# Performance work log

Hardware: AMD Instinct MI355X
Metric: run time of the kernel (lower is better)

## Reference

```python
import jax, jax.numpy as jnp
import numpy as np

BBOX_MIN = jnp.array([0.6, 0.6, 0.2], dtype=jnp.float32)
BBOX_MAX = jnp.array([-0.8, -1.2, -0.2], dtype=jnp.float32)
# level resolutions: floor(16 * (4096/16)**(l/15)) for l in 0..4
RES = [16, 23, 33, 48, 70]
OFFS = np.cumsum([0] + [(r + 1) ** 3 for r in RES]).tolist()  # dense grids fit in 2^21 hashmap


def _encode(x, table):
    # x: [N,3] in [0,1]; table: [533601, 2] concatenated dense per-level grids
    feats = []
    for l, r in enumerate(RES):
        g = r + 1  # grid points per axis
        pos = x * r
        p0 = jnp.clip(jnp.floor(pos), 0.0, r - 1)
        f = pos - p0  # trilinear weights, [N,3]
        p0 = p0.astype(jnp.int32)
        acc = jnp.zeros((x.shape[0], 2), dtype=table.dtype)
        for dx in (0, 1):
            for dy in (0, 1):
                for dz in (0, 1):
                    idx = ((p0[:, 0] + dx) * g + (p0[:, 1] + dy)) * g + (p0[:, 2] + dz) + OFFS[l]
                    wx = f[:, 0] if dx else 1.0 - f[:, 0]
                    wy = f[:, 1] if dy else 1.0 - f[:, 1]
                    wz = f[:, 2] if dz else 1.0 - f[:, 2]
                    acc = acc + (wx * wy * wz)[:, None] * table[idx]
        feats.append(acc)
    return jnp.concatenate(feats, axis=-1)  # [N, 10]


def setup_inputs() -> dict:
    key = jax.random.key(0)
    ks = jax.random.split(key, 5)
    T = OFFS[-1]  # 533601
    return {
        "texc": jax.random.uniform(ks[0], (2048, 2048, 3), dtype=jnp.float32),
        "table": jax.random.normal(ks[1], (T, 2), dtype=jnp.float32) * 1e-4,
        "W0": jax.random.normal(ks[2], (32, 10), dtype=jnp.float32) * (2.0 / 10) ** 0.5,
        "W1": jax.random.normal(ks[3], (32, 32), dtype=jnp.float32) * (2.0 / 32) ** 0.5,
        "W2": jax.random.normal(ks[4], (3, 32), dtype=jnp.float32) * (2.0 / 32) ** 0.5,
        "min_val": jnp.zeros((3,), jnp.float32),
        "max_val": jnp.ones((3,), jnp.float32),
        "frame_id": 0,
    }


def reference(texc, table, W0, W1, W2, min_val, max_val, frame_id):
    x = texc.reshape(-1, 3)
    # coordinate normalization into [0,1] with hardcoded bbox (as in source)
    x = jnp.clip((x - BBOX_MIN) / (BBOX_MAX - BBOX_MIN), 0.0, 1.0)
    p = _encode(x, table)              # [N, 10]
    h = jax.nn.relu(p @ W0.T)          # [N, 32]
    h = jax.nn.relu(h @ W1.T)          # [N, 32]
    o = h @ W2.T                       # [N, 3]
    o = jax.nn.sigmoid(o) * (max_val - min_val) + min_val
    return o.reshape(*texc.shape[:-1], 3)
```

## Files before the change

kernel.cpp:

```cpp
#include <hip/hip_runtime.h>
#include <hip/hip_bf16.h>
#include <math.h>


namespace {

typedef __attribute__((ext_vector_type(8)))  short short8;
typedef __attribute__((ext_vector_type(16))) float f32x16;
typedef __attribute__((ext_vector_type(4), aligned(8))) float f32x4a;
typedef __attribute__((ext_vector_type(4), aligned(16))) unsigned int u32x4;

union S8 { short8 v; int d[4]; };

#define SWAP32(a, b) asm volatile("v_permlane32_swap_b32 %0, %1" : "+v"(a), "+v"(b))

constexpr int RES0 = 16, RES1 = 23, RES2 = 33, RES3 = 48, RES4 = 70;
constexpr int TOFF0 = 0, TOFF1 = 4913, TOFF2 = 18737, TOFF3 = 58041, TOFF4 = 175690;
constexpr int COFF0 = 0;
constexpr int COFF1 = COFF0 + RES0*RES0*RES0;
constexpr int COFF2 = COFF1 + RES1*RES1*RES1;
constexpr int COFF3 = COFF2 + RES2*RES2*RES2;
constexpr int COFF4 = COFF3 + RES3*RES3*RES3;
constexpr int NCELL = COFF4 + RES4*RES4*RES4;
constexpr size_t WS_NEED = (size_t)NCELL * 32u;

__device__ __forceinline__ int cvt_pk(float lo, float hi) {
    int d;
    asm("v_cvt_pk_bf16_f32 %0, %1, %2" : "=v"(d) : "v"(lo), "v"(hi));
    return d;
}

__device__ __forceinline__ short8 pack8(float4 a, float4 b) {
    S8 u;
    u.d[0] = cvt_pk(a.x, a.y);
    u.d[1] = cvt_pk(a.z, a.w);
    u.d[2] = cvt_pk(b.x, b.y);
    u.d[3] = cvt_pk(b.z, b.w);
    return u.v;
}

__device__ __forceinline__ float clamp01(float v) {
    return fminf(fmaxf(v, 0.0f), 1.0f);
}

__device__ __forceinline__ float2 upk(unsigned int u) {
    float2 r;
    r.x = __uint_as_float(u << 16);
    r.y = __uint_as_float(u & 0xffff0000u);
    return r;
}

__device__ __forceinline__ void marshal_h(const f32x16& acc, short8& k0, short8& k1) {
    int q[8];
    #pragma unroll
    for (int j = 0; j < 8; ++j) {
        float lo = fmaxf(acc[2*j],   0.0f);
        float hi = fmaxf(acc[2*j+1], 0.0f);
        q[j] = cvt_pk(lo, hi);
    }
    int a0 = q[0], b0 = q[2]; SWAP32(a0, b0);
    int a1 = q[1], b1 = q[3]; SWAP32(a1, b1);
    int a2 = q[4], b2 = q[6]; SWAP32(a2, b2);
    int a3 = q[5], b3 = q[7]; SWAP32(a3, b3);
    S8 u0; u0.d[0] = a0; u0.d[1] = a1; u0.d[2] = b0; u0.d[3] = b1; k0 = u0.v;
    S8 u1; u1.d[0] = a2; u1.d[1] = a3; u1.d[2] = b2; u1.d[3] = b3; k1 = u1.v;
}

__global__ __launch_bounds__(256) void prep_kernel(
    const float* __restrict__ table, unsigned int* __restrict__ ws)
{
    int ci = blockIdx.x * blockDim.x + threadIdx.x;
    if (ci >= NCELL) return;

    int r, toff, c0;
    if      (ci < COFF1) { r = RES0; toff = TOFF0; c0 = COFF0; }
    else if (ci < COFF2) { r = RES1; toff = TOFF1; c0 = COFF1; }
    else if (ci < COFF3) { r = RES2; toff = TOFF2; c0 = COFF2; }
    else if (ci < COFF4) { r = RES3; toff = TOFF3; c0 = COFF3; }
    else                 { r = RES4; toff = TOFF4; c0 = COFF4; }

    int lc = ci - c0;
    int cz = lc % r;
    int t  = lc / r;
    int cy = t % r;
    int cx = t / r;
    int g  = r + 1;

    const float2* tab2 = reinterpret_cast<const float2*>(table);
    int base = (cx * g + cy) * g + cz + toff;

    unsigned int* dst = ws + (size_t)ci * 8;
    #pragma unroll
    for (int dx = 0; dx < 2; ++dx) {
        #pragma unroll
        for (int dy = 0; dy < 2; ++dy) {
            #pragma unroll
            for (int dz = 0; dz < 2; ++dz) {
                float2 v = tab2[base + (dx * g + dy) * g + dz];
                dst[dx*4 + dy*2 + dz] = (unsigned int)cvt_pk(v.x, v.y);
            }
        }
    }
}

template<bool USE_WS>
__global__ __launch_bounds__(512) void mlptex_kernel(
    const float* __restrict__ texc,
    const float* __restrict__ table,
    const unsigned int* __restrict__ cells,
    const float* __restrict__ W0,
    const float* __restrict__ W1,
    const float* __restrict__ W2,
    const float* __restrict__ minv,
    const float* __restrict__ maxv,
    float* __restrict__ out,
    int N)
{
    const int tid  = blockIdx.x * blockDim.x + threadIdx.x;
    const int lane = threadIdx.x & 63;
    const int pt   = min(tid, N - 1);
    const bool live = (tid < N);

    const int row = lane & 31;
    const int kb  = lane >> 5;

    short8 w0f, w1f0, w1f1;
    {
        const float* p0 = W0 + row * 10;
        float4 a, b;
        if (kb == 0) {
            float2 f0 = *(const float2*)(p0 + 0);
            float2 f1 = *(const float2*)(p0 + 2);
            float2 f2 = *(const float2*)(p0 + 4);
            float2 f3 = *(const float2*)(p0 + 6);
            a = make_float4(f0.x, f0.y, f1.x, f1.y);
            b = make_float4(f2.x, f2.y, f3.x, f3.y);
        } else {
            float2 f4 = *(const float2*)(p0 + 8);
            a = make_float4(f4.x, f4.y, 0.f, 0.f);
            b = make_float4(0.f, 0.f, 0.f, 0.f);
        }
        w0f = pack8(a, b);

        const float* p1 = W1 + row * 32 + kb * 8;
        w1f0 = pack8(*(const float4*)(p1),      *(const float4*)(p1 + 4));
        w1f1 = pack8(*(const float4*)(p1 + 16), *(const float4*)(p1 + 20));
    }
    short8 w2f0 = {0,0,0,0,0,0,0,0}, w2f1 = {0,0,0,0,0,0,0,0};
    if (row < 3) {
        const float* p2 = W2 + row * 32 + kb * 8;
        w2f0 = pack8(*(const float4*)(p2),      *(const float4*)(p2 + 4));
        w2f1 = pack8(*(const float4*)(p2 + 16), *(const float4*)(p2 + 20));
    }

    const float* tp = texc + 3 * pt;
    float x = __builtin_nontemporal_load(tp + 0);
    float y = __builtin_nontemporal_load(tp + 1);
    float z = __builtin_nontemporal_load(tp + 2);
    x = clamp01((x - 0.6f) * (-1.0f/1.4f));
    y = clamp01((y - 0.6f) * (-1.0f/1.8f));
    z = clamp01((z - 0.2f) * (-1.0f/0.4f));

    const int RESL[5]  = {RES0, RES1, RES2, RES3, RES4};
    const int TOFFL[5] = {TOFF0, TOFF1, TOFF2, TOFF3, TOFF4};
    const int COFFL[5] = {COFF0, COFF1, COFF2, COFF3, COFF4};
    const float2* tab2 = reinterpret_cast<const float2*>(table);

    float pf[10];
    #pragma unroll
    for (int l = 0; l < 5; ++l) {
        const int r = RESL[l];
        const int g = r + 1;
        const float rf = (float)r;
        float px = x * rf, py = y * rf, pz = z * rf;
        float fx = fminf(floorf(px), rf - 1.0f);
        float fy = fminf(floorf(py), rf - 1.0f);
        float fz = fminf(floorf(pz), rf - 1.0f);
        float tx = px - fx, ty = py - fy, tz = pz - fz;
        int ix = (int)fx & 127, iy = (int)fy & 127, iz = (int)fz & 127;

        float sx = 1.0f - tx, sy = 1.0f - ty, sz = 1.0f - tz;
        float w00 = sy*sz, w01 = sy*tz, w10 = ty*sz, w11 = ty*tz;
        float a00 = sx*w00, a01 = sx*w01, a10 = sx*w10, a11 = sx*w11;
        float b00 = tx*w00, b01 = tx*w01, b10 = tx*w10, b11 = tx*w11;

        float f0, f1;
        if constexpr (USE_WS) {
            int ci = (ix * r + iy) * r + iz + COFFL[l];
            const u32x4* cp = reinterpret_cast<const u32x4*>(cells + (size_t)ci * 8);
            u32x4 lo = cp[0];
            u32x4 hi = cp[1];
            float2 c000 = upk(lo.x), c001 = upk(lo.y), c010 = upk(lo.z), c011 = upk(lo.w);
            float2 c100 = upk(hi.x), c101 = upk(hi.y), c110 = upk(hi.z), c111 = upk(hi.w);
            f0  = a00*c000.x;            f1  = a00*c000.y;
            f0  = fmaf(a01, c001.x, f0); f1  = fmaf(a01, c001.y, f1);
            f0  = fmaf(a10, c010.x, f0); f1  = fmaf(a10, c010.y, f1);
            f0  = fmaf(a11, c011.x, f0); f1  = fmaf(a11, c011.y, f1);
            f0  = fmaf(b00, c100.x, f0); f1  = fmaf(b00, c100.y, f1);
            f0  = fmaf(b01, c101.x, f0); f1  = fmaf(b01, c101.y, f1);
            f0  = fmaf(b10, c110.x, f0); f1  = fmaf(b10, c110.y, f1);
            f0  = fmaf(b11, c111.x, f0); f1  = fmaf(b11, c111.y, f1);
        } else {
            const int gg = g * g;
            int base = (ix * g + iy) * g + iz + TOFFL[l];
            f32x4a q00 = *reinterpret_cast<const f32x4a*>(tab2 + base);
            f32x4a q01 = *reinterpret_cast<const f32x4a*>(tab2 + base + g);
            f32x4a q10 = *reinterpret_cast<const f32x4a*>(tab2 + base + gg);
            f32x4a q11 = *reinterpret_cast<const f32x4a*>(tab2 + base + gg + g);
            f0  = a00*q00[0];            f1  = a00*q00[1];
            f0  = fmaf(a01, q00[2], f0); f1  = fmaf(a01, q00[3], f1);
            f0  = fmaf(a10, q01[0], f0); f1  = fmaf(a10, q01[1], f1);
            f0  = fmaf(a11, q01[2], f0); f1  = fmaf(a11, q01[3], f1);
            f0  = fmaf(b00, q10[0], f0); f1  = fmaf(b00, q10[1], f1);
            f0  = fmaf(b01, q10[2], f0); f1  = fmaf(b01, q10[3], f1);
            f0  = fmaf(b10, q11[0], f0); f1  = fmaf(b10, q11[1], f1);
            f0  = fmaf(b11, q11[2], f0); f1  = fmaf(b11, q11[3], f1);
        }
        pf[2*l+0] = f0;
        pf[2*l+1] = f1;
    }

    int pk0 = cvt_pk(pf[0], pf[1]);
    int pk1 = cvt_pk(pf[2], pf[3]);
    int pk2 = cvt_pk(pf[4], pf[5]);
    int pk3 = cvt_pk(pf[6], pf[7]);
    int pk4 = cvt_pk(pf[8], pf[9]);

    int n1d0 = pk0, n2d0 = pk4; SWAP32(n1d0, n2d0);
    int n1d1 = pk1, n2d1 = 0;   SWAP32(n1d1, n2d1);
    int n1d2 = pk2, n2d2 = 0;   SWAP32(n1d2, n2d2);
    int n1d3 = pk3, n2d3 = 0;   SWAP32(n1d3, n2d3);
    S8 ub1; ub1.d[0]=n1d0; ub1.d[1]=n1d1; ub1.d[2]=n1d2; ub1.d[3]=n1d3;
    S8 ub2; ub2.d[0]=n2d0; ub2.d[1]=n2d1; ub2.d[2]=n2d2; ub2.d[3]=n2d3;

    const f32x16 zero16 = {0.f,0.f,0.f,0.f,0.f,0.f,0.f,0.f,
                           0.f,0.f,0.f,0.f,0.f,0.f,0.f,0.f};

    f32x16 h0a = __builtin_amdgcn_mfma_f32_32x32x16_bf16(w0f, ub1.v, zero16, 0, 0, 0);
    f32x16 h0b = __builtin_amdgcn_mfma_f32_32x32x16_bf16(w0f, ub2.v, zero16, 0, 0, 0);

    short8 h0a_k0, h0a_k1, h0b_k0, h0b_k1;
    marshal_h(h0a, h0a_k0, h0a_k1);
    marshal_h(h0b, h0b_k0, h0b_k1);

    f32x16 h1a = __builtin_amdgcn_mfma_f32_32x32x16_bf16(w1f0, h0a_k0, zero16, 0, 0, 0);
    h1a = __builtin_amdgcn_mfma_f32_32x32x16_bf16(w1f1, h0a_k1, h1a, 0, 0, 0);
    f32x16 h1b = __builtin_amdgcn_mfma_f32_32x32x16_bf16(w1f0, h0b_k0, zero16, 0, 0, 0);
    h1b = __builtin_amdgcn_mfma_f32_32x32x16_bf16(w1f1, h0b_k1, h1b, 0, 0, 0);

    short8 h1a_k0, h1a_k1, h1b_k0, h1b_k1;
    marshal_h(h1a, h1a_k0, h1a_k1);
    marshal_h(h1b, h1b_k0, h1b_k1);

    f32x16 oa = __builtin_amdgcn_mfma_f32_32x32x16_bf16(w2f0, h1a_k0, zero16, 0, 0, 0);
    oa = __builtin_amdgcn_mfma_f32_32x32x16_bf16(w2f1, h1a_k1, oa, 0, 0, 0);
    f32x16 ob = __builtin_amdgcn_mfma_f32_32x32x16_bf16(w2f0, h1b_k0, zero16, 0, 0, 0);
    ob = __builtin_amdgcn_mfma_f32_32x32x16_bf16(w2f1, h1b_k1, ob, 0, 0, 0);

    float mn[3] = {minv[0], minv[1], minv[2]};
    float sc[3] = {maxv[0] - minv[0], maxv[1] - minv[1], maxv[2] - minv[2]};

    float o[3];
    #pragma unroll
    for (int j = 0; j < 3; ++j) {
        float t0 = ob[j], t1 = ob[j];
        SWAP32(t0, t1);
        float v = (lane < 32) ? oa[j] : t0;
        float s = 1.0f / (1.0f + __expf(-v));
        o[j] = fmaf(s, sc[j], mn[j]);
    }

    if (live) {
        float* op = out + 3 * tid;
        __builtin_nontemporal_store(o[0], op + 0);
        __builtin_nontemporal_store(o[1], op + 1);
        __builtin_nontemporal_store(o[2], op + 2);
    }
}

}

extern "C" void kernel_launch(void* const* d_in, const int* in_sizes, int n_in,
                              void* d_out, int out_size, void* d_ws, size_t ws_size,
                              hipStream_t stream) {
    const float* texc  = (const float*)d_in[0];
    const float* table = (const float*)d_in[1];
    const float* W0    = (const float*)d_in[2];
    const float* W1    = (const float*)d_in[3];
    const float* W2    = (const float*)d_in[4];
    const float* minv  = (const float*)d_in[5];
    const float* maxv  = (const float*)d_in[6];
    float* out = (float*)d_out;

    const int N = in_sizes[0] / 3;
    const int threads = 512;
    const int blocks = (N + threads - 1) / threads;

    if (ws_size >= WS_NEED) {
        unsigned int* cells = (unsigned int*)d_ws;
        prep_kernel<<<(NCELL + 255) / 256, 256, 0, stream>>>(table, cells);
        mlptex_kernel<true><<<blocks, threads, 0, stream>>>(
            texc, table, cells, W0, W1, W2, minv, maxv, out, N);
    } else {
        mlptex_kernel<false><<<blocks, threads, 0, stream>>>(
            texc, table, nullptr, W0, W1, W2, minv, maxv, out, N);
    }
}
```

Before: 222.0 us.

## Process two points per thread and vectorize prep kernel with per-level templates

The main kernel now handles two points per thread, one from each half of the input. Each thread runs two encode passes and two MLP chains, which gives more independent gathers and MFMA work per thread to hide latency and amortizes the weight fragment setup. The prep kernel is templated per level so the divides use constants, and it uses 16-byte loads and nontemporal vector stores. This assumes N is even; an odd N would leave the last point unwritten, and register pressure rises.

```diff
diff --git a/kernel.cpp b/kernel.cpp
--- a/kernel.cpp
+++ b/kernel.cpp
@@ -7,7 +7,7 @@
 
 typedef __attribute__((ext_vector_type(8)))  short short8;
 typedef __attribute__((ext_vector_type(16))) float f32x16;
-typedef __attribute__((ext_vector_type(4), aligned(8))) float f32x4a;
+typedef __attribute__((ext_vector_type(4), aligned(8)))  float f32x4a;
 typedef __attribute__((ext_vector_type(4), aligned(16))) unsigned int u32x4;
 
 union S8 { short8 v; int d[4]; };
@@ -66,107 +66,59 @@
     S8 u1; u1.d[0] = a2; u1.d[1] = a3; u1.d[2] = b2; u1.d[3] = b3; k1 = u1.v;
 }
 
+template<int R, int TOFF, int COFF>
+__device__ __forceinline__ void prep_level(int ci, const float2* __restrict__ tab2,
+                                           unsigned int* __restrict__ ws)
+{
+    constexpr int G = R + 1;
+    int lc = ci - COFF;
+    int cz = lc % R;
+    int t  = lc / R;
+    int cy = t % R;
+    int cx = t / R;
+    int base = (cx * G + cy) * G + cz + TOFF;
+
+    f32x4a q00 = *reinterpret_cast<const f32x4a*>(tab2 + base);
+    f32x4a q01 = *reinterpret_cast<const f32x4a*>(tab2 + base + G);
+    f32x4a q10 = *reinterpret_cast<const f32x4a*>(tab2 + base + G*G);
+    f32x4a q11 = *reinterpret_cast<const f32x4a*>(tab2 + base + G*G + G);
+
+    u32x4 lo, hi;
+    lo.x = (unsigned int)cvt_pk(q00[0], q00[1]);
+    lo.y = (unsigned int)cvt_pk(q00[2], q00[3]);
+    lo.z = (unsigned int)cvt_pk(q01[0], q01[1]);
+    lo.w = (unsigned int)cvt_pk(q01[2], q01[3]);
+    hi.x = (unsigned int)cvt_pk(q10[0], q10[1]);
+    hi.y = (unsigned int)cvt_pk(q10[2], q10[3]);
+    hi.z = (unsigned int)cvt_pk(q11[0], q11[1]);
+    hi.w = (unsigned int)cvt_pk(q11[2], q11[3]);
+
+    u32x4* dst = reinterpret_cast<u32x4*>(ws + (size_t)ci * 8);
+    __builtin_nontemporal_store(lo, dst);
+    __builtin_nontemporal_store(hi, dst + 1);
+}
+
 __global__ __launch_bounds__(256) void prep_kernel(
     const float* __restrict__ table, unsigned int* __restrict__ ws)
 {
     int ci = blockIdx.x * blockDim.x + threadIdx.x;
-    if (ci >= NCELL) return;
-
-    int r, toff, c0;
-    if      (ci < COFF1) { r = RES0; toff = TOFF0; c0 = COFF0; }
-    else if (ci < COFF2) { r = RES1; toff = TOFF1; c0 = COFF1; }
-    else if (ci < COFF3) { r = RES2; toff = TOFF2; c0 = COFF2; }
-    else if (ci < COFF4) { r = RES3; toff = TOFF3; c0 = COFF3; }
-    else                 { r = RES4; toff = TOFF4; c0 = COFF4; }
-
-    int lc = ci - c0;
-    int cz = lc % r;
-    int t  = lc / r;
-    int cy = t % r;
-    int cx = t / r;
-    int g  = r + 1;
-
     const float2* tab2 = reinterpret_cast<const float2*>(table);
-    int base = (cx * g + cy) * g + cz + toff;
-
-    unsigned int* dst = ws + (size_t)ci * 8;
-    #pragma unroll
-    for (int dx = 0; dx < 2; ++dx) {
-        #pragma unroll
-        for (int dy = 0; dy < 2; ++dy) {
-            #pragma unroll
-            for (int dz = 0; dz < 2; ++dz) {
-                float2 v = tab2[base + (dx * g + dy) * g + dz];
-                dst[dx*4 + dy*2 + dz] = (unsigned int)cvt_pk(v.x, v.y);
-            }
-        }
-    }
+    if      (ci < COFF1) prep_level<RES0, TOFF0, COFF0>(ci, tab2, ws);
+    else if (ci < COFF2) prep_level<RES1, TOFF1, COFF1>(ci, tab2, ws);
+    else if (ci < COFF3) prep_level<RES2, TOFF2, COFF2>(ci, tab2, ws);
+    else if (ci < COFF4) prep_level<RES3, TOFF3, COFF3>(ci, tab2, ws);
+    else if (ci < NCELL) prep_level<RES4, TOFF4, COFF4>(ci, tab2, ws);
 }
 
 template<bool USE_WS>
-__global__ __launch_bounds__(512) void mlptex_kernel(
-    const float* __restrict__ texc,
-    const float* __restrict__ table,
-    const unsigned int* __restrict__ cells,
-    const float* __restrict__ W0,
-    const float* __restrict__ W1,
-    const float* __restrict__ W2,
-    const float* __restrict__ minv,
-    const float* __restrict__ maxv,
-    float* __restrict__ out,
-    int N)
-{
-    const int tid  = blockIdx.x * blockDim.x + threadIdx.x;
-    const int lane = threadIdx.x & 63;
-    const int pt   = min(tid, N - 1);
-    const bool live = (tid < N);
-
-    const int row = lane & 31;
-    const int kb  = lane >> 5;
-
-    short8 w0f, w1f0, w1f1;
-    {
-        const float* p0 = W0 + row * 10;
-        float4 a, b;
-        if (kb == 0) {
-            float2 f0 = *(const float2*)(p0 + 0);
-            float2 f1 = *(const float2*)(p0 + 2);
-            float2 f2 = *(const float2*)(p0 + 4);
-            float2 f3 = *(const float2*)(p0 + 6);
-            a = make_float4(f0.x, f0.y, f1.x, f1.y);
-            b = make_float4(f2.x, f2.y, f3.x, f3.y);
-        } else {
-            float2 f4 = *(const float2*)(p0 + 8);
-            a = make_float4(f4.x, f4.y, 0.f, 0.f);
-            b = make_float4(0.f, 0.f, 0.f, 0.f);
-        }
-        w0f = pack8(a, b);
-
-        const float* p1 = W1 + row * 32 + kb * 8;
-        w1f0 = pack8(*(const float4*)(p1),      *(const float4*)(p1 + 4));
-        w1f1 = pack8(*(const float4*)(p1 + 16), *(const float4*)(p1 + 20));
-    }
-    short8 w2f0 = {0,0,0,0,0,0,0,0}, w2f1 = {0,0,0,0,0,0,0,0};
-    if (row < 3) {
-        const float* p2 = W2 + row * 32 + kb * 8;
-        w2f0 = pack8(*(const float4*)(p2),      *(const float4*)(p2 + 4));
-        w2f1 = pack8(*(const float4*)(p2 + 16), *(const float4*)(p2 + 20));
-    }
-
-    const float* tp = texc + 3 * pt;
-    float x = __builtin_nontemporal_load(tp + 0);
-    float y = __builtin_nontemporal_load(tp + 1);
-    float z = __builtin_nontemporal_load(tp + 2);
-    x = clamp01((x - 0.6f) * (-1.0f/1.4f));
-    y = clamp01((y - 0.6f) * (-1.0f/1.8f));
-    z = clamp01((z - 0.2f) * (-1.0f/0.4f));
-
+__device__ __forceinline__ void encode(float x, float y, float z,
+    const unsigned int* __restrict__ cells, const float2* __restrict__ tab2,
+    float* __restrict__ pf)
+{
     const int RESL[5]  = {RES0, RES1, RES2, RES3, RES4};
     const int TOFFL[5] = {TOFF0, TOFF1, TOFF2, TOFF3, TOFF4};
     const int COFFL[5] = {COFF0, COFF1, COFF2, COFF3, COFF4};
-    const float2* tab2 = reinterpret_cast<const float2*>(table);
-
-    float pf[10];
+
     #pragma unroll
     for (int l = 0; l < 5; ++l) {
         const int r = RESL[l];
@@ -219,7 +171,12 @@
         pf[2*l+0] = f0;
         pf[2*l+1] = f1;
     }
-
+}
+
+__device__ __forceinline__ void run_mlp(const float* __restrict__ pf,
+    short8 w0f, short8 w1f0, short8 w1f1, short8 w2f0, short8 w2f1,
+    int lane, float* __restrict__ v)
+{
     int pk0 = cvt_pk(pf[0], pf[1]);
     int pk1 = cvt_pk(pf[2], pf[3]);
     int pk2 = cvt_pk(pf[4], pf[5]);
@@ -257,24 +214,104 @@
     f32x16 ob = __builtin_amdgcn_mfma_f32_32x32x16_bf16(w2f0, h1b_k0, zero16, 0, 0, 0);
     ob = __builtin_amdgcn_mfma_f32_32x32x16_bf16(w2f1, h1b_k1, ob, 0, 0, 0);
 
-    float mn[3] = {minv[0], minv[1], minv[2]};
-    float sc[3] = {maxv[0] - minv[0], maxv[1] - minv[1], maxv[2] - minv[2]};
-
-    float o[3];
     #pragma unroll
     for (int j = 0; j < 3; ++j) {
         float t0 = ob[j], t1 = ob[j];
         SWAP32(t0, t1);
-        float v = (lane < 32) ? oa[j] : t0;
-        float s = 1.0f / (1.0f + __expf(-v));
-        o[j] = fmaf(s, sc[j], mn[j]);
-    }
+        v[j] = (lane < 32) ? oa[j] : t0;
+    }
+}
+
+template<bool USE_WS>
+__global__ __launch_bounds__(512) void mlptex_kernel(
+    const float* __restrict__ texc,
+    const float* __restrict__ table,
+    const unsigned int* __restrict__ cells,
+    const float* __restrict__ W0,
+    const float* __restrict__ W1,
+    const float* __restrict__ W2,
+    const float* __restrict__ minv,
+    const float* __restrict__ maxv,
+    float* __restrict__ out,
+    int N)
+{
+    const int H   = N >> 1;
+    const int tid = blockIdx.x * blockDim.x + threadIdx.x;
+    const int lane = threadIdx.x & 63;
+    const int pt0 = min(tid, H - 1);
+    const int pt1 = pt0 + H;
+    const bool live = (tid < H);
+
+    const int row = lane & 31;
+    const int kb  = lane >> 5;
+
+    short8 w0f, w1f0, w1f1;
+    {
+        const float* p0 = W0 + row * 10;
+        float4 a, b;
+        if (kb == 0) {
+            float2 f0 = *(const float2*)(p0 + 0);
+            float2 f1 = *(const float2*)(p0 + 2);
+            float2 f2 = *(const float2*)(p0 + 4);
+            float2 f3 = *(const float2*)(p0 + 6);
+            a = make_float4(f0.x, f0.y, f1.x, f1.y);
+            b = make_float4(f2.x, f2.y, f3.x, f3.y);
+        } else {
+            float2 f4 = *(const float2*)(p0 + 8);
+            a = make_float4(f4.x, f4.y, 0.f, 0.f);
+            b = make_float4(0.f, 0.f, 0.f, 0.f);
+        }
+        w0f = pack8(a, b);
+
+        const float* p1 = W1 + row * 32 + kb * 8;
+        w1f0 = pack8(*(const float4*)(p1),      *(const float4*)(p1 + 4));
+        w1f1 = pack8(*(const float4*)(p1 + 16), *(const float4*)(p1 + 20));
+    }
+    short8 w2f0 = {0,0,0,0,0,0,0,0}, w2f1 = {0,0,0,0,0,0,0,0};
+    if (row < 3) {
+        const float* p2 = W2 + row * 32 + kb * 8;
+        w2f0 = pack8(*(const float4*)(p2),      *(const float4*)(p2 + 4));
+        w2f1 = pack8(*(const float4*)(p2 + 16), *(const float4*)(p2 + 20));
+    }
+
+    const float* ta = texc + 3 * pt0;
+    const float* tb = texc + 3 * pt1;
+    float x0 = __builtin_nontemporal_load(ta + 0);
+    float y0 = __builtin_nontemporal_load(ta + 1);
+    float z0 = __builtin_nontemporal_load(ta + 2);
+    float x1 = __builtin_nontemporal_load(tb + 0);
+    float y1 = __builtin_nontemporal_load(tb + 1);
+    float z1 = __builtin_nontemporal_load(tb + 2);
+    x0 = clamp01((x0 - 0.6f) * (-1.0f/1.4f));
+    y0 = clamp01((y0 - 0.6f) * (-1.0f/1.8f));
+    z0 = clamp01((z0 - 0.2f) * (-1.0f/0.4f));
+    x1 = clamp01((x1 - 0.6f) * (-1.0f/1.4f));
+    y1 = clamp01((y1 - 0.6f) * (-1.0f/1.8f));
+    z1 = clamp01((z1 - 0.2f) * (-1.0f/0.4f));
+
+    const float2* tab2 = reinterpret_cast<const float2*>(table);
+
+    float pf0[10], pf1[10];
+    encode<USE_WS>(x0, y0, z0, cells, tab2, pf0);
+    encode<USE_WS>(x1, y1, z1, cells, tab2, pf1);
+
+    float v0[3], v1[3];
+    run_mlp(pf0, w0f, w1f0, w1f1, w2f0, w2f1, lane, v0);
+    run_mlp(pf1, w0f, w1f0, w1f1, w2f0, w2f1, lane, v1);
+
+    float mn[3] = {minv[0], minv[1], minv[2]};
+    float sc[3] = {maxv[0] - minv[0], maxv[1] - minv[1], maxv[2] - minv[2]};
 
     if (live) {
-        float* op = out + 3 * tid;
-        __builtin_nontemporal_store(o[0], op + 0);
-        __builtin_nontemporal_store(o[1], op + 1);
-        __builtin_nontemporal_store(o[2], op + 2);
+        float* oa = out + 3 * pt0;
+        float* ob = out + 3 * pt1;
+        #pragma unroll
+        for (int j = 0; j < 3; ++j) {
+            float s0 = 1.0f / (1.0f + __expf(-v0[j]));
+            float s1 = 1.0f / (1.0f + __expf(-v1[j]));
+            __builtin_nontemporal_store(fmaf(s0, sc[j], mn[j]), oa + j);
+            __builtin_nontemporal_store(fmaf(s1, sc[j], mn[j]), ob + j);
+        }
     }
 }
 
@@ -294,7 +331,7 @@
 
     const int N = in_sizes[0] / 3;
     const int threads = 512;
-    const int blocks = (N + threads - 1) / threads;
+    const int blocks = ((N / 2) + threads - 1) / threads;
 
     if (ws_size >= WS_NEED) {
         unsigned int* cells = (unsigned int*)d_ws;
```

Measured after the change: 204.1 us. -8.1%, faster.
